# Optimization experiments

Hardware: AMD Instinct MI355X
Metric: run time of the kernel (lower is better)

Reference implementation:

```python
import jax, jax.numpy as jnp
import numpy as np

T, B, H = 1024, 256, 20


def setup_inputs() -> dict:
    key = jax.random.key(0)
    ks = jax.random.split(key, 6)

    def lin_w(k, fan_in, fan_out):
        bound = 1.0 / np.sqrt(fan_in)
        return jax.random.uniform(k, (fan_in, fan_out), jnp.float32, -bound, bound)

    # t is time-reversed (torch.flip): strictly decreasing, so dt = t[0]-t[1] > 0
    t = jnp.linspace(1.0, 0.0, T, dtype=jnp.float32).reshape(T, 1)
    y = jax.random.uniform(ks[0], (B, 1, 3), jnp.float32)  # initial SIR state per batch
    return {
        "t": t,
        "y": y,
        "w1": lin_w(ks[1], 1, H), "b1": jnp.zeros((H,), jnp.float32),
        "w2": lin_w(ks[2], H, H), "b2": jnp.zeros((H,), jnp.float32),
        "w3": lin_w(ks[3], H, H), "b3": jnp.zeros((H,), jnp.float32),
        "w4": lin_w(ks[4], H, 1), "b4": jnp.zeros((1,), jnp.float32),
        "beta": jnp.asarray(0.2, jnp.float32),
        "gamma": jnp.asarray(0.2, jnp.float32),
    }


def reference(t, y, w1, b1, w2, b2, w3, b3, w4, b4, beta, gamma):
    Tn = t.shape[0]
    dt = t[0, 0] - t[1, 0]  # positive scalar (t is reversed)

    # memory kernel me(t): Linear-Tanh x3 -> Linear-Sigmoid, shape [T]
    h = jnp.tanh(t @ w1 + b1)
    h = jnp.tanh(h @ w2 + b2)
    h = jnp.tanh(h @ w3 + b3)
    me = jax.nn.sigmoid(h @ w4 + b4)[:, 0]  # [T]
    # pad so me[-j:] can be read as a fixed-length dynamic slice (zeros past end)
    me_pad = jnp.concatenate([me, jnp.zeros((Tn,), me.dtype)])  # [2T]

    y0 = jnp.transpose(y, (1, 0, 2))[0]  # [B,3]  (y.transpose(1,0) then first/only row)
    Bn = y0.shape[0]
    # history buffer of I-compartment values; entries >= current length stay zero
    I_hist0 = jnp.zeros((Tn, Bn), y0.dtype).at[0].set(y0[:, 1])

    def step(carry, idx):
        y_cur, I_hist = carry  # y_cur [B,3], I_hist [T,B]
        j = idx + 1  # current solution length
        # kernel slice w[k] = me[T - j + k]; for k >= j both w (padding) and I_hist are 0
        w = jax.lax.dynamic_slice(me_pad, (Tn - j,), (Tn,))  # [T]
        integ = dt * jnp.einsum('t,tb->b', w, I_hist)  # memory integral, [B]
        S, I = y_cur[:, 0], y_cur[:, 1]
        bSI = beta * S * I
        gI = gamma * I
        d = jnp.stack([-bSI + integ, bSI - gI, gI - integ], axis=1)  # [B,3]
        y_next = y_cur + d * dt  # forward Euler
        I_hist = I_hist.at[j].set(y_next[:, 1])
        return (y_next, I_hist), (d, y_next)

    (_, _), (ds, ys) = jax.lax.scan(step, (y0, I_hist0), jnp.arange(Tn - 1))
    solution = jnp.concatenate([y0[None], ys], axis=0)  # [T,B,3]
    # original leaves diff[T-1] as zeros (loop fills rows 0..T-2)
    diff = jnp.concatenate([ds, jnp.zeros((1, Bn, 3), ds.dtype)], axis=0)  # [T,B,3]
    return solution, diff
```

## Files before the change

### kernel.cpp

```cpp
#include <hip/hip_runtime.h>

#define T_N 1024
#define B_N 256
#define H_N 20
#define NW  8
#define NDW (NW - 1)
#define SIH 1096

typedef _Float16 h8_t __attribute__((ext_vector_type(8)));

#if __has_builtin(__builtin_amdgcn_fdot2)
#define DOT8(acc, mv, iv)                                                           \
    acc = __builtin_amdgcn_fdot2(__builtin_shufflevector(mv, mv, 0, 1),             \
                                 __builtin_shufflevector(iv, iv, 0, 1), acc, false);\
    acc = __builtin_amdgcn_fdot2(__builtin_shufflevector(mv, mv, 2, 3),             \
                                 __builtin_shufflevector(iv, iv, 2, 3), acc, false);\
    acc = __builtin_amdgcn_fdot2(__builtin_shufflevector(mv, mv, 4, 5),             \
                                 __builtin_shufflevector(iv, iv, 4, 5), acc, false);\
    acc = __builtin_amdgcn_fdot2(__builtin_shufflevector(mv, mv, 6, 7),             \
                                 __builtin_shufflevector(iv, iv, 6, 7), acc, false);
#else
#define DOT8(acc, mv, iv)                                                           \
    _Pragma("unroll")                                                               \
    for (int _k = 0; _k < 8; ++_k) acc = fmaf((float)mv[_k], (float)iv[_k], acc);
#endif

__device__ __forceinline__ float rdlane_i(float v, int lane) {
    return __uint_as_float((unsigned)__builtin_amdgcn_readlane((int)__float_as_uint(v), lane));
}
__device__ __forceinline__ float fast_tanh(float x) {
    const float e = __expf(2.0f * x);
    return fmaf(-2.0f, __builtin_amdgcn_rcpf(e + 1.0f), 1.0f);
}
__device__ __forceinline__ float fast_sigmoid(float x) {
    return __builtin_amdgcn_rcpf(1.0f + __expf(-x));
}

#define REP64(F) \
    F(0) F(1) F(2) F(3) F(4) F(5) F(6) F(7) F(8) F(9) F(10) F(11) F(12) F(13) \
    F(14) F(15) F(16) F(17) F(18) F(19) F(20) F(21) F(22) F(23) F(24) F(25)   \
    F(26) F(27) F(28) F(29) F(30) F(31) F(32) F(33) F(34) F(35) F(36) F(37)   \
    F(38) F(39) F(40) F(41) F(42) F(43) F(44) F(45) F(46) F(47) F(48) F(49)   \
    F(50) F(51) F(52) F(53) F(54) F(55) F(56) F(57) F(58) F(59) F(60) F(61)   \
    F(62) F(63)

__global__ __launch_bounds__(512, 1) void scan_kernel(
    const float* __restrict__ t,
    const float* __restrict__ y,
    const float* __restrict__ w1, const float* __restrict__ b1,
    const float* __restrict__ w2, const float* __restrict__ b2,
    const float* __restrict__ w3, const float* __restrict__ b3,
    const float* __restrict__ w4, const float* __restrict__ b4,
    const float* __restrict__ beta_p,
    const float* __restrict__ gamma_p,
    float* __restrict__ out)
{
    __shared__ __align__(16) float    sMeF[T_N];
    __shared__ __align__(16) _Float16 sMeH[T_N];
    __shared__ __align__(16) _Float16 sIhR[8 * SIH];
    __shared__ float P[2][NDW][64];

    const int b   = blockIdx.x;
    const int tid = threadIdx.x;
    const int wid = tid >> 6;
    const int L   = tid & 63;

    const int f    = (-L) & 7;
    const int R8   = L + f;
    const int row  = L & 7;
    const int iofs = row * SIH + (f ? 0 : 8);

    if (tid < 64) sIhR[(tid >> 3) * SIH + (tid & 7)] = (_Float16)0.0f;

#pragma unroll
    for (int v = 0; v < 2; ++v) {
        const int mi = tid + v * 512;
        const float x = t[mi];

        float h1[H_N], h2[H_N];
#pragma unroll
        for (int k = 0; k < H_N; ++k) h1[k] = fast_tanh(fmaf(x, w1[k], b1[k]));

#pragma unroll 4
        for (int k = 0; k < H_N; ++k) {
            float a = b2[k];
#pragma unroll
            for (int j = 0; j < H_N; ++j) a = fmaf(h1[j], w2[j * H_N + k], a);
            h2[k] = fast_tanh(a);
        }

        float a4 = b4[0];
#pragma unroll 4
        for (int k = 0; k < H_N; ++k) {
            float a = b3[k];
#pragma unroll
            for (int j = 0; j < H_N; ++j) a = fmaf(h2[j], w3[j * H_N + k], a);
            a4 = fmaf(fast_tanh(a), w4[k], a4);
        }

        const float meval = fast_sigmoid(a4);
        sMeF[mi] = meval;
        sMeH[mi] = (_Float16)meval;
    }

    const float dt    = t[0] - t[1];
    const float beta  = beta_p[0];
    const float gma   = gamma_p[0];
    const float invdt = 1.0f / dt;

    const float S0 = y[b * 3 + 0];
    const float I0 = y[b * 3 + 1];
    const float R0 = y[b * 3 + 2];
    const float TOT = S0 + I0 + R0;

    if (tid < 8) sIhR[tid * SIH + 8 - tid] = (_Float16)I0;

    float* __restrict__ diff = out + (size_t)T_N * B_N * 3;
    if (tid < 3) diff[((size_t)(T_N - 1) * B_N + b) * 3 + tid] = 0.0f;

    __syncthreads();

    float mf[7];
#pragma unroll
    for (int d = 1; d <= 7; ++d) mf[d - 1] = sMeF[T_N - 64 - L - d];

    const float dtb  = dt * beta;
    const float ndtg = -dt * gma;
    const float dt2  = dt * dt;
    const float meT1 = sMeF[T_N - 1];

    float S = S0, I = I0, oS = S0, oI = I0;
    float acc_cur = 0.0f, acc_nxt = 0.0f, pre = 0.0f;
    float carryS = S0, carryI = I0;

#define TBLDECL(k) float rm_##k, rn_##k;
    REP64(TBLDECL)
#undef TBLDECL
    if (wid == 0) {
#define TBLINIT(k)                                                      \
        rm_##k = ((k) < L) ? sMeF[T_N - L + (k)] : 0.0f;                \
        rn_##k = sMeF[T_N - 64 - L + (k)];
        REP64(TBLINIT)
#undef TBLINIT
    }

#define STEPB(M_, FIRST_)                                               \
    {                                                                   \
        const float sum = (FIRST_) ? pre : fmaf(meT1, I, pre);          \
        float pnx = pre;                                                \
        if ((M_) < 63) pnx = rdlane_i(acc_cur, (M_) + 1);               \
        const float bI = dtb * I;                                       \
        const float i1 = fmaf(ndtg, I, I);                              \
        const float q  = bI * S;                                        \
        const float s1 = S - q;                                         \
        S = fmaf(dt2, sum, s1);                                         \
        I = i1 + q;                                                     \
        const bool cap = (L == (M_));                                   \
        oS = cap ? S : oS;                                              \
        oI = cap ? I : oI;                                              \
        acc_cur = fmaf(rm_##M_, I, acc_cur);                            \
        acc_nxt = fmaf(rn_##M_, I, acc_nxt);                            \
        pre = pnx;                                                      \
    }
#define STEP_GE1(M_) if ((M_) >= 1) STEPB(M_, false)
#define STEP_GE2(M_) if ((M_) >= 2) STEPB(M_, false)

    for (int c = 0; c < 16; ++c) {
        if (wid == 0) {
            if (c == 0) {
                acc_cur = rm_0 * I;
                acc_nxt = rn_0 * I;
                pre = rdlane_i(acc_cur, 1);
                STEPB(1, true)
                REP64(STEP_GE2)
            } else {
                float ac = acc_nxt;
#pragma unroll
                for (int w = 0; w < NDW; ++w) ac += P[c & 1][w][L];
                acc_cur = ac;
                acc_nxt = 0.0f;
                pre = rdlane_i(acc_cur, 0);
                STEPB(0, true)
                REP64(STEP_GE1)
            }

            const int j = 64 * c + L;
            const _Float16 hI = (_Float16)oI;
#pragma unroll
            for (int r = 0; r < 8; ++r) sIhR[r * SIH + 8 + (j - r)] = hI;

            const float oR = TOT - oS - oI;
            const size_t so = ((size_t)j * B_N + b) * 3;
            out[so + 0] = oS;
            out[so + 1] = oI;
            out[so + 2] = oR;

            float sm1 = __shfl_up(oS, 1);
            float im1 = __shfl_up(oI, 1);
            if (L == 0) { sm1 = carryS; im1 = carryI; }
            if (j > 0) {
                const float d0 = (oS - sm1) * invdt;
                const float d1 = (oI - im1) * invdt;
                const float d2 = -d0 - d1;
                const size_t dofs = ((size_t)(j - 1) * B_N + b) * 3;
                diff[dofs + 0] = d0;
                diff[dofs + 1] = d1;
                diff[dofs + 2] = d2;
            }
            carryS = rdlane_i(oS, 63);
            carryI = rdlane_i(oI, 63);
        } else if (c < 15) {
            const int w    = wid - 1;
            const int G    = 8 * c;
            const int idx0 = (T_N - 64 * (c + 1)) - R8;
            float p0 = 0.0f, p1 = 0.0f;
            int s = w;
            for (; s + NDW < G; s += 2 * NDW) {
                const h8_t mv0 = *(const h8_t*)&sMeH[idx0 + 8 * s];
                const h8_t iv0 = *(const h8_t*)&sIhR[iofs + 8 * s];
                const h8_t mv1 = *(const h8_t*)&sMeH[idx0 + 8 * (s + NDW)];
                const h8_t iv1 = *(const h8_t*)&sIhR[iofs + 8 * (s + NDW)];
                DOT8(p0, mv0, iv0)
                DOT8(p1, mv1, iv1)
            }
            if (s < G) {
                const h8_t mv0 = *(const h8_t*)&sMeH[idx0 + 8 * s];
                const h8_t iv0 = *(const h8_t*)&sIhR[iofs + 8 * s];
                DOT8(p0, mv0, iv0)
            }
            float p = p0 + p1;
            if (w == 0) {
#pragma unroll
                for (int d = 1; d <= 7; ++d) {
                    const float ih = (float)sIhR[8 + 64 * c - d];
                    if (d <= f) p = fmaf(mf[d - 1], ih, p);
                }
            }
            P[(c + 1) & 1][w][L] = p;
        }
        __syncthreads();
    }
#undef STEPB
#undef STEP_GE1
#undef STEP_GE2
}

extern "C" void kernel_launch(void* const* d_in, const int* in_sizes, int n_in,
                              void* d_out, int out_size, void* d_ws, size_t ws_size,
                              hipStream_t stream) {
    const float* t     = (const float*)d_in[0];
    const float* y     = (const float*)d_in[1];
    const float* w1    = (const float*)d_in[2];
    const float* b1    = (const float*)d_in[3];
    const float* w2    = (const float*)d_in[4];
    const float* b2    = (const float*)d_in[5];
    const float* w3    = (const float*)d_in[6];
    const float* b3    = (const float*)d_in[7];
    const float* w4    = (const float*)d_in[8];
    const float* b4    = (const float*)d_in[9];
    const float* beta  = (const float*)d_in[10];
    const float* gamma = (const float*)d_in[11];

    scan_kernel<<<B_N, 512, 0, stream>>>(t, y, w1, b1, w2, b2, w3, b3, w4, b4,
                                         beta, gamma, (float*)d_out);
}
```

Measured before the change: 121.6 us.

## Replace per-lane 128-register kernel tables with DPP-shifted rotating weights

Drops the 128 per-lane unrolled weight registers (rm/rn tables) and instead keeps one memory-kernel weight per lane, shifting it one lane each step with a DPP wave_shr. The weight that falls off lane 63 of the current table is injected into lane 0 of the next table. This frees a large block of VGPRs and removes the deferred lookahead 'pre' term, so the sum now comes directly from a readlane of the updated accumulator. In exchange each serial step gains a DPP move, a readlane and a select on the critical dependency chain.

```diff
diff --git a/kernel.cpp b/kernel.cpp
--- a/kernel.cpp
+++ b/kernel.cpp
@@ -6,6 +6,7 @@
 #define NW  8
 #define NDW (NW - 1)
 #define SIH 1096
+#define DPP_WAVE_SHR1 0x138
 
 typedef _Float16 h8_t __attribute__((ext_vector_type(8)));
 
@@ -36,6 +37,17 @@
     return __builtin_amdgcn_rcpf(1.0f + __expf(-x));
 }
 
+#if __has_builtin(__builtin_amdgcn_update_dpp)
+__device__ __forceinline__ int shift1z(int v, int ) {
+    return __builtin_amdgcn_update_dpp(0, v, DPP_WAVE_SHR1, 0xF, 0xF, false);
+}
+#else
+__device__ __forceinline__ int shift1z(int v, int L) {
+    const int s = __shfl_up(v, 1);
+    return (L == 0) ? 0 : s;
+}
+#endif
+
 #define REP64(F) \
     F(0) F(1) F(2) F(3) F(4) F(5) F(6) F(7) F(8) F(9) F(10) F(11) F(12) F(13) \
     F(14) F(15) F(16) F(17) F(18) F(19) F(20) F(21) F(22) F(23) F(24) F(25)   \
@@ -127,28 +139,18 @@
     const float dtb  = dt * beta;
     const float ndtg = -dt * gma;
     const float dt2  = dt * dt;
-    const float meT1 = sMeF[T_N - 1];
 
     float S = S0, I = I0, oS = S0, oI = I0;
-    float acc_cur = 0.0f, acc_nxt = 0.0f, pre = 0.0f;
+    float acc_cur = 0.0f, acc_nxt = 0.0f, sum = 0.0f;
     float carryS = S0, carryI = I0;
-
-#define TBLDECL(k) float rm_##k, rn_##k;
-    REP64(TBLDECL)
-#undef TBLDECL
-    if (wid == 0) {
-#define TBLINIT(k)                                                      \
-        rm_##k = ((k) < L) ? sMeF[T_N - L + (k)] : 0.0f;                \
-        rn_##k = sMeF[T_N - 64 - L + (k)];
-        REP64(TBLINIT)
-#undef TBLINIT
-    }
-
-#define STEPB(M_, FIRST_)                                               \
+    const bool lane0 = (L == 0);
+
+    const int g0i = (L > 0) ? __float_as_int(sMeF[T_N - L]) : 0;
+    const int h0i = __float_as_int(sMeF[T_N - 64 - L]);
+    int gri = g0i, hri = h0i;
+
+#define STEPB(M_)                                                       \
     {                                                                   \
-        const float sum = (FIRST_) ? pre : fmaf(meT1, I, pre);          \
-        float pnx = pre;                                                \
-        if ((M_) < 63) pnx = rdlane_i(acc_cur, (M_) + 1);               \
         const float bI = dtb * I;                                       \
         const float i1 = fmaf(ndtg, I, I);                              \
         const float q  = bI * S;                                        \
@@ -158,30 +160,41 @@
         const bool cap = (L == (M_));                                   \
         oS = cap ? S : oS;                                              \
         oI = cap ? I : oI;                                              \
-        acc_cur = fmaf(rm_##M_, I, acc_cur);                            \
-        acc_nxt = fmaf(rn_##M_, I, acc_nxt);                            \
-        pre = pnx;                                                      \
+        if ((M_) < 63) {                                                \
+            const int inj = __builtin_amdgcn_readlane(gri, 63);         \
+            acc_cur = fmaf(__int_as_float(gri), I, acc_cur);            \
+            acc_nxt = fmaf(__int_as_float(hri), I, acc_nxt);            \
+            sum = rdlane_i(acc_cur, (M_) + 1);                          \
+            gri = shift1z(gri, L);                                      \
+            const int hsh = shift1z(hri, L);                            \
+            hri = lane0 ? inj : hsh;                                    \
+        } else {                                                        \
+            acc_nxt = fmaf(__int_as_float(hri), I, acc_nxt);            \
+        }                                                               \
     }
-#define STEP_GE1(M_) if ((M_) >= 1) STEPB(M_, false)
-#define STEP_GE2(M_) if ((M_) >= 2) STEPB(M_, false)
+#define STEP_GE1(M_) if ((M_) >= 1) STEPB(M_)
 
     for (int c = 0; c < 16; ++c) {
         if (wid == 0) {
+            gri = g0i;
+            hri = h0i;
             if (c == 0) {
-                acc_cur = rm_0 * I;
-                acc_nxt = rn_0 * I;
-                pre = rdlane_i(acc_cur, 1);
-                STEPB(1, true)
-                REP64(STEP_GE2)
+                const int inj = __builtin_amdgcn_readlane(gri, 63);
+                acc_cur = __int_as_float(gri) * I;
+                acc_nxt = __int_as_float(hri) * I;
+                sum = rdlane_i(acc_cur, 1);
+                gri = shift1z(gri, L);
+                const int hsh = shift1z(hri, L);
+                hri = lane0 ? inj : hsh;
+                REP64(STEP_GE1)
             } else {
                 float ac = acc_nxt;
 #pragma unroll
                 for (int w = 0; w < NDW; ++w) ac += P[c & 1][w][L];
                 acc_cur = ac;
                 acc_nxt = 0.0f;
-                pre = rdlane_i(acc_cur, 0);
-                STEPB(0, true)
-                REP64(STEP_GE1)
+                sum = rdlane_i(acc_cur, 0);
+                REP64(STEPB)
             }
 
             const int j = 64 * c + L;
@@ -242,7 +255,6 @@
     }
 #undef STEPB
 #undef STEP_GE1
-#undef STEP_GE2
 }
 
 extern "C" void kernel_launch(void* const* d_in, const int* in_sizes, int n_in,
```

Result: slower. 133.1 us (+9.5%).

## Replace per-lane kernel weight tables with DPP shifts and move bridge dot to wave 0

Applied to the files above, without the earlier changes.

Drops the two 64-entry register tables of memory-kernel weights. Each lane now holds one weight and passes it to its neighbour with a DPP wave shift on every step, and the next-chunk accumulator is replaced by a separate bridge dot product that wave 0 computes from shared memory after each chunk. The Euler update is also rewritten algebraically to shorten the serial dependency chain, and the boundary-correction FMAs move from helper wave 1 into wave 0's bridge. This sharply cuts register pressure on wave 0, but adds a cross-lane DPP op per step on the critical serial chain and extra serial work for wave 0 between chunks.

```diff
diff --git a/kernel.cpp b/kernel.cpp
--- a/kernel.cpp
+++ b/kernel.cpp
@@ -6,6 +6,7 @@
 #define NW  8
 #define NDW (NW - 1)
 #define SIH 1096
+#define DPP_WAVE_SHR1 0x138
 
 typedef _Float16 h8_t __attribute__((ext_vector_type(8)));
 
@@ -36,6 +37,17 @@
     return __builtin_amdgcn_rcpf(1.0f + __expf(-x));
 }
 
+#if __has_builtin(__builtin_amdgcn_update_dpp)
+__device__ __forceinline__ int shift1z(int v, int ) {
+    return __builtin_amdgcn_update_dpp(0, v, DPP_WAVE_SHR1, 0xF, 0xF, false);
+}
+#else
+__device__ __forceinline__ int shift1z(int v, int L) {
+    const int s = __shfl_up(v, 1);
+    return (L == 0) ? 0 : s;
+}
+#endif
+
 #define REP64(F) \
     F(0) F(1) F(2) F(3) F(4) F(5) F(6) F(7) F(8) F(9) F(10) F(11) F(12) F(13) \
     F(14) F(15) F(16) F(17) F(18) F(19) F(20) F(21) F(22) F(23) F(24) F(25)   \
@@ -120,66 +132,62 @@
 
     __syncthreads();
 
-    float mf[7];
-#pragma unroll
-    for (int d = 1; d <= 7; ++d) mf[d - 1] = sMeF[T_N - 64 - L - d];
+    float mf2[7];
+#pragma unroll
+    for (int d = 1; d <= 7; ++d) mf2[d - 1] = sMeF[T_N - L - d];
 
     const float dtb  = dt * beta;
-    const float ndtg = -dt * gma;
+    const float ndtb = -dtb;
+    const float cI   = 1.0f - dt * gma;
     const float dt2  = dt * dt;
     const float meT1 = sMeF[T_N - 1];
+    const float k2   = dt2 * meT1;
 
     float S = S0, I = I0, oS = S0, oI = I0;
-    float acc_cur = 0.0f, acc_nxt = 0.0f, pre = 0.0f;
+    float acc_cur = 0.0f, pre = 0.0f, dt2p = 0.0f, bridge = 0.0f;
     float carryS = S0, carryI = I0;
 
-#define TBLDECL(k) float rm_##k, rn_##k;
-    REP64(TBLDECL)
-#undef TBLDECL
-    if (wid == 0) {
-#define TBLINIT(k)                                                      \
-        rm_##k = ((k) < L) ? sMeF[T_N - L + (k)] : 0.0f;                \
-        rn_##k = sMeF[T_N - 64 - L + (k)];
-        REP64(TBLINIT)
-#undef TBLINIT
-    }
+    const int g0i = (L > 0) ? __float_as_int(sMeF[T_N - L]) : 0;
+    int gri = g0i;
 
 #define STEPB(M_, FIRST_)                                               \
     {                                                                   \
-        const float sum = (FIRST_) ? pre : fmaf(meT1, I, pre);          \
+        const float t2s = (FIRST_) ? dt2p : fmaf(k2, I, dt2p);          \
         float pnx = pre;                                                \
         if ((M_) < 63) pnx = rdlane_i(acc_cur, (M_) + 1);               \
-        const float bI = dtb * I;                                       \
-        const float i1 = fmaf(ndtg, I, I);                              \
-        const float q  = bI * S;                                        \
-        const float s1 = S - q;                                         \
-        S = fmaf(dt2, sum, s1);                                         \
-        I = i1 + q;                                                     \
+        const float wS = fmaf(ndtb, I, 1.0f);                           \
+        const float u  = fmaf(dtb, S, cI);                              \
+        const float Sn = fmaf(S, wS, t2s);                              \
+        I = u * I;                                                      \
+        S = Sn;                                                         \
         const bool cap = (L == (M_));                                   \
         oS = cap ? S : oS;                                              \
         oI = cap ? I : oI;                                              \
-        acc_cur = fmaf(rm_##M_, I, acc_cur);                            \
-        acc_nxt = fmaf(rn_##M_, I, acc_nxt);                            \
+        acc_cur = fmaf(__int_as_float(gri), I, acc_cur);                \
+        gri = shift1z(gri, L);                                          \
         pre = pnx;                                                      \
+        dt2p = dt2 * pnx;                                               \
     }
 #define STEP_GE1(M_) if ((M_) >= 1) STEPB(M_, false)
 #define STEP_GE2(M_) if ((M_) >= 2) STEPB(M_, false)
 
     for (int c = 0; c < 16; ++c) {
         if (wid == 0) {
+            gri = g0i;
             if (c == 0) {
-                acc_cur = rm_0 * I;
-                acc_nxt = rn_0 * I;
+                acc_cur = __int_as_float(gri) * I;
                 pre = rdlane_i(acc_cur, 1);
+                dt2p = dt2 * pre;
+                gri = shift1z(gri, L);
                 STEPB(1, true)
                 REP64(STEP_GE2)
             } else {
-                float ac = acc_nxt;
+                float ac = bridge;
 #pragma unroll
                 for (int w = 0; w < NDW; ++w) ac += P[c & 1][w][L];
                 acc_cur = ac;
-                acc_nxt = 0.0f;
                 pre = rdlane_i(acc_cur, 0);
+                dt2p = dt2 * pre;
                 STEPB(0, true)
                 REP64(STEP_GE1)
             }
@@ -209,6 +217,26 @@
             }
             carryS = rdlane_i(oS, 63);
             carryI = rdlane_i(oI, 63);
+
+            if (c < 15) {
+                const int idx0b = (T_N - 64 * (c + 1)) - R8;
+                float bp = 0.0f;
+#pragma unroll
+                for (int sg = 0; sg < 8; ++sg) {
+                    const int s = 8 * c + sg;
+                    const h8_t mv = *(const h8_t*)&sMeH[idx0b + 8 * s];
+                    const h8_t iv = *(const h8_t*)&sIhR[iofs + 8 * s];
+                    DOT8(bp, mv, iv)
+                }
+#pragma unroll
+                for (int d = 1; d <= 7; ++d) {
+                    if (d <= f) {
+                        const float ih = (float)sIhR[8 + 64 * (c + 1) - d];
+                        bp = fmaf(mf2[d - 1], ih, bp);
+                    }
+                }
+                bridge = bp;
+            }
         } else if (c < 15) {
             const int w    = wid - 1;
             const int G    = 8 * c;
@@ -228,15 +256,7 @@
                 const h8_t iv0 = *(const h8_t*)&sIhR[iofs + 8 * s];
                 DOT8(p0, mv0, iv0)
             }
-            float p = p0 + p1;
-            if (w == 0) {
-#pragma unroll
-                for (int d = 1; d <= 7; ++d) {
-                    const float ih = (float)sIhR[8 + 64 * c - d];
-                    if (d <= f) p = fmaf(mf[d - 1], ih, p);
-                }
-            }
-            P[(c + 1) & 1][w][L] = p;
+            P[(c + 1) & 1][w][L] = p0 + p1;
         }
         __syncthreads();
     }
```

Result: slower. 125.8 us (+3.5%).
